# Kernel optimization log

Hardware: AMD Instinct MI355X
Metric: run time of the kernel (lower is better)

## Reference

```python
import jax, jax.numpy as jnp
import numpy as np

N = 50000        # nodes
E = 800000       # edges (before self loops)
NFEAT = 128
HEADS = 8
NHID = 16
SLOPE = 0.2      # PyG GATConv default negative_slope


def gat_conv(x, src, dst, W, a_src, a_dst, bias, heads, out_ch, concat):
    n = x.shape[0]
    h = (x @ W).reshape(n, heads, out_ch)                 # [N,H,C]
    al_s = jnp.sum(h * a_src, axis=-1)                    # [N,H]
    al_d = jnp.sum(h * a_dst, axis=-1)                    # [N,H]
    # add self loops (PyG GATConv default add_self_loops=True)
    loop = jnp.arange(n, dtype=src.dtype)
    s = jnp.concatenate([src, loop])
    d = jnp.concatenate([dst, loop])
    e = jax.nn.leaky_relu(al_s[s] + al_d[d], SLOPE)       # [E+N,H]
    # numerically stable softmax over incoming edges of each dst node
    emax = jax.lax.stop_gradient(jax.ops.segment_max(e, d, num_segments=n))
    ex = jnp.exp(e - emax[d])
    denom = jax.ops.segment_sum(ex, d, num_segments=n)
    alpha = ex / denom[d]                                 # [E+N,H]
    out = jax.ops.segment_sum(h[s] * alpha[:, :, None], d, num_segments=n)  # [N,H,C]
    out = out.reshape(n, heads * out_ch) if concat else out.mean(axis=1)
    return out + bias


def setup_inputs() -> dict:
    key = jax.random.key(0)
    ks = jax.random.split(key, 11)
    x = jax.random.normal(ks[0], (N, NFEAT), jnp.float32)
    src = jax.random.randint(ks[1], (E,), 0, N, dtype=jnp.int32)
    dst = jax.random.randint(ks[2], (E,), 0, N, dtype=jnp.int32)
    dst = jnp.where(src == dst, (dst + 1) % N, dst)  # no pre-existing self loops
    edge_index = jnp.stack([src, dst])
    sc = 0.1
    W1 = jax.random.normal(ks[3], (NFEAT, HEADS * NHID), jnp.float32) * sc
    a_src1 = jax.random.normal(ks[4], (HEADS, NHID), jnp.float32) * sc
    a_dst1 = jax.random.normal(ks[5], (HEADS, NHID), jnp.float32) * sc
    b1 = jnp.zeros((HEADS * NHID,), jnp.float32)
    W2 = jax.random.normal(ks[6], (HEADS * NHID, NHID), jnp.float32) * sc
    a_src2 = jax.random.normal(ks[7], (1, NHID), jnp.float32) * sc
    a_dst2 = jax.random.normal(ks[8], (1, NHID), jnp.float32) * sc
    b2 = jnp.zeros((NHID,), jnp.float32)
    return {"x": x, "edge_index": edge_index, "W1": W1, "a_src1": a_src1,
            "a_dst1": a_dst1, "b1": b1, "W2": W2, "a_src2": a_src2,
            "a_dst2": a_dst2, "b2": b2}


def reference(x, edge_index, W1, a_src1, a_dst1, b1, W2, a_src2, a_dst2, b2):
    src, dst = edge_index[0], edge_index[1]
    # layer 1: GATConv(nfeat -> nhid, heads=8, concat) + relu (dropout off in eval)
    h = jax.nn.relu(gat_conv(x, src, dst, W1, a_src1, a_dst1, b1, HEADS, NHID, True))
    # layer 2: GATConv(heads*nhid -> nhid, heads=1, concat=False) + relu
    out = jax.nn.relu(gat_conv(h, src, dst, W2, a_src2, a_dst2, b2, 1, NHID, False))
    return out
```

## Files before the change

kernel.cpp:

```cpp
#include <hip/hip_runtime.h>

#define NFEAT 128
#define HEADS 8
#define NHID 16
#define SLOPE 0.2f
#define BSH 8
#define CAPSH 13

typedef __fp16 f16x8 __attribute__((ext_vector_type(8)));
typedef __fp16 f16x2 __attribute__((ext_vector_type(2)));
typedef float  f4v   __attribute__((ext_vector_type(4)));

__device__ __forceinline__ unsigned pack2h(float a, float b) {
    union { f16x2 h; unsigned u; } r;
    r.h = __builtin_amdgcn_cvt_pkrtz(a, b);
    return r.u;
}
__device__ __forceinline__ f16x2 as_f16x2(unsigned u) {
    union { unsigned u; f16x2 h; } r; r.u = u; return r.h;
}
__device__ __forceinline__ f16x8 frag_from_f32(const float* p) {
    float4 q0 = *(const float4*)p;
    float4 q1 = *(const float4*)(p + 4);
    union { f16x8 v; f16x2 h[4]; } r;
    r.h[0] = __builtin_amdgcn_cvt_pkrtz(q0.x, q0.y);
    r.h[1] = __builtin_amdgcn_cvt_pkrtz(q0.z, q0.w);
    r.h[2] = __builtin_amdgcn_cvt_pkrtz(q1.x, q1.y);
    r.h[3] = __builtin_amdgcn_cvt_pkrtz(q1.z, q1.w);
    return r.v;
}


__global__ __launch_bounds__(256) void k_bscatter(const int* __restrict__ src,
                                                  const int* __restrict__ dst,
                                                  int E, int chunk,
                                                  int* __restrict__ bcount,
                                                  unsigned* __restrict__ pairs) {
    __shared__ int cnt[256], base[256];
    int t = threadIdx.x;
    int beg = blockIdx.x * chunk;
    int end = min(beg + chunk, E);
    if (beg >= end) return;
    cnt[t] = 0;
    __syncthreads();
    for (int i = beg + t; i < end; i += 256)
        atomicAdd(&cnt[dst[i] >> BSH], 1);
    __syncthreads();
    int c = cnt[t];
    base[t] = c ? (atomicAdd(&bcount[t], c) + (t << CAPSH)) : 0;
    __syncthreads();
    cnt[t] = 0;
    __syncthreads();
    for (int i = beg + t; i < end; i += 256) {
        int d = dst[i];
        int b = d >> BSH;
        int ofs = atomicAdd(&cnt[b], 1);
        pairs[base[b] + ofs] = (unsigned)src[i] | ((unsigned)(d & 255) << 16);
    }
}


__global__ __launch_bounds__(256) void k_scan_prep(const int* __restrict__ bcount,
                                                   int* __restrict__ cstart,
                                                   int* __restrict__ row_start,
                                                   int E, int n,
                                                   const float* __restrict__ W1,
                                                   const float* __restrict__ as1,
                                                   const float* __restrict__ ad1,
                                                   const float* __restrict__ W2,
                                                   unsigned* __restrict__ Wt1,
                                                   __fp16* __restrict__ Aat1,
                                                   unsigned* __restrict__ W2t) {
    if (blockIdx.x == 0) {
        __shared__ int sh[256];
        int t = threadIdx.x;
        int nb = (n + 255) >> BSH;
        int v = (t < nb) ? bcount[t] : 0;
        sh[t] = v;
        __syncthreads();
        for (int off = 1; off < 256; off <<= 1) {
            int u = (t >= off) ? sh[t - off] : 0;
            __syncthreads();
            sh[t] += u;
            __syncthreads();
        }
        cstart[t] = sh[t] - v;
        if (t == 0) row_start[n] = E + n;
        return;
    }
    int t = (blockIdx.x - 1) * 256 + threadIdx.x;
    if (t < 8192) {
        int c = t >> 6, m = t & 63;
        int k = 2 * m;
        Wt1[t] = pack2h(W1[k * 128 + c], W1[(k + 1) * 128 + c]);
    } else if (t < 10240) {
        int idx = t - 8192;
        int j = idx >> 7, k = idx & 127;
        float v = 0.f;
        if (j < 8)  { if ((k >> 4) == j)     v = as1[k]; }
        else        { if ((k >> 4) == j - 8) v = ad1[k]; }
        Aat1[idx] = (__fp16)v;
    } else if (t < 11264) {
        int idx = t - 10240;
        int c = idx >> 6, m = idx & 63;
        int k = 2 * m;
        W2t[idx] = pack2h(W2[k * 16 + c], W2[(k + 1) * 16 + c]);
    }
}


__global__ __launch_bounds__(256) void k_csr_gemm1(const unsigned* __restrict__ pairs,
                                                   const int* __restrict__ bcount,
                                                   const int* __restrict__ cstart,
                                                   int* __restrict__ row_start,
                                                   unsigned short* __restrict__ csr,
                                                   const float* __restrict__ xf,
                                                   const __fp16* __restrict__ Wt,
                                                   const __fp16* __restrict__ Aat,
                                                   unsigned* __restrict__ h1u,
                                                   float* __restrict__ als,
                                                   float* __restrict__ ald,
                                                   int n, int nbuck) {
    __shared__ unsigned smem[4][32 * 64];
    if ((int)blockIdx.x < nbuck) {
        int* deg = (int*)&smem[0][0];
        int* sc  = deg + 256;
        int b = blockIdx.x, t = threadIdx.x;
        int d0 = b << BSH;
        int nd = min(256, n - d0);
        deg[t] = (t < nd) ? 1 : 0;
        __syncthreads();
        int pbeg = b << CAPSH, pend = pbeg + bcount[b];
        for (int i = pbeg + t; i < pend; i += 256)
            atomicAdd(&deg[(pairs[i] >> 16) & 255], 1);
        __syncthreads();
        int v = deg[t];
        sc[t] = v;
        __syncthreads();
        for (int off = 1; off < 256; off <<= 1) {
            int u = (t >= off) ? sc[t - off] : 0;
            __syncthreads();
            sc[t] += u;
            __syncthreads();
        }
        int excl = sc[t] - v;
        int cbase = cstart[b] + d0;
        if (t < nd) row_start[d0 + t] = cbase + excl;
        __syncthreads();
        deg[t] = excl;
        __syncthreads();
        if (t < nd) {
            int pos = atomicAdd(&deg[t], 1);
            csr[cbase + pos] = (unsigned short)(d0 + t);
        }
        for (int i = pbeg + t; i < pend; i += 256) {
            unsigned p = pairs[i];
            int pos = atomicAdd(&deg[(p >> 16) & 255], 1);
            csr[cbase + pos] = (unsigned short)(p & 0xFFFFu);
        }
        return;
    }
    int bid = blockIdx.x - nbuck;
    int tid = threadIdx.x;
    int w = tid >> 6, l = tid & 63;
    int l15 = l & 15, lq = l >> 4;
    int wbase = bid * 128 + w * 32;
    f4v acc[2][8] = {};
    int r0 = min(wbase + l15, n - 1);
    int r1 = min(wbase + 16 + l15, n - 1);
#pragma unroll
    for (int kb = 0; kb < 4; ++kb) {
        int ko = kb * 32 + lq * 8;
        f16x8 a0 = frag_from_f32(&xf[(size_t)r0 * 128 + ko]);
        f16x8 a1 = frag_from_f32(&xf[(size_t)r1 * 128 + ko]);
#pragma unroll
        for (int cg = 0; cg < 8; ++cg) {
            f16x8 b = *(const f16x8*)&Wt[(size_t)(cg * 16 + l15) * 128 + ko];
            acc[0][cg] = __builtin_amdgcn_mfma_f32_16x16x32_f16(a0, b, acc[0][cg], 0, 0, 0);
            acc[1][cg] = __builtin_amdgcn_mfma_f32_16x16x32_f16(a1, b, acc[1][cg], 0, 0, 0);
        }
    }
    unsigned* myl = smem[w];
#pragma unroll
    for (int T = 0; T < 2; ++T) {
#pragma unroll
        for (int cg = 0; cg < 8; ++cg) {
#pragma unroll
            for (int j = 0; j < 4; ++j) {
                float v = acc[T][cg][j];
                float vo = __shfl_xor(v, 1);
                if ((l15 & 1) == 0) {
                    int nd = T * 16 + lq * 4 + j;
                    int wd = cg * 8 + (l15 >> 1);
                    int widx = nd * 64 + (((wd >> 2) ^ (nd & 15)) << 2) + (wd & 3);
                    myl[widx] = pack2h(v, vo);
                }
            }
        }
    }
    __syncthreads();
#pragma unroll
    for (int it = 0; it < 8; ++it) {
        int nd = it * 4 + lq;
        int node = wbase + nd;
        uint4 vv = *(const uint4*)&myl[nd * 64 + ((l15 ^ (nd & 15)) << 2)];
        if (node < n) *(uint4*)&h1u[(size_t)node * 64 + l15 * 4] = vv;
    }
#pragma unroll
    for (int T = 0; T < 2; ++T) {
        f4v acca = {};
#pragma unroll
        for (int kb = 0; kb < 4; ++kb) {
            int nd = T * 16 + l15;
            f16x8 ah = *(const f16x8*)&myl[nd * 64 + (((kb * 4 + lq) ^ (nd & 15)) << 2)];
            f16x8 bb = *(const f16x8*)&Aat[l15 * 128 + kb * 32 + lq * 8];
            acca = __builtin_amdgcn_mfma_f32_16x16x32_f16(ah, bb, acca, 0, 0, 0);
        }
#pragma unroll
        for (int j = 0; j < 4; ++j) {
            int node = wbase + T * 16 + lq * 4 + j;
            if (node < n) {
                if (l15 < 8) als[(size_t)node * 8 + l15] = acca[j];
                else         ald[(size_t)node * 8 + (l15 - 8)] = acca[j];
            }
        }
    }
}


__global__ __launch_bounds__(256) void k_agg1(const unsigned* __restrict__ hu,
                                              const float* __restrict__ als,
                                              const float* __restrict__ ald,
                                              const float* __restrict__ bias,
                                              const int* __restrict__ row_start,
                                              const unsigned short* __restrict__ csr,
                                              unsigned* __restrict__ out1u, int n) {
    int t = threadIdx.x;
    int w = t >> 6;
    int l = t & 63;
    int lc = l & 3;
    int es = (l >> 2) & 3;
    int ns = l >> 4;
    int g = blockIdx.x & 3;
    int nn = (blockIdx.x >> 2) * 16 + w * 4 + ns;
    if (nn >= n) return;
    const unsigned* hg = hu + g * 16;
    int hd = g * 2 + (lc >> 1);
    float aldv = ald[(size_t)nn * 8 + hd];
    int beg = row_start[nn], end = row_start[nn + 1];
    int len = end - beg;
    int g0 = beg + ((len * es) >> 2);
    int g1 = beg + ((len * (es + 1)) >> 2);
    float a[8] = {0.f, 0.f, 0.f, 0.f, 0.f, 0.f, 0.f, 0.f};
    float dn = 0.f;
    f16x2 one2; one2[0] = (__fp16)1.f; one2[1] = (__fp16)1.f;
    int i = g0;
    for (; i + 4 <= g1; i += 4) {
        int s0 = csr[i], s1 = csr[i + 1], s2 = csr[i + 2], s3 = csr[i + 3];
        float e0 = als[(size_t)s0 * 8 + hd];
        float e1 = als[(size_t)s1 * 8 + hd];
        float e2 = als[(size_t)s2 * 8 + hd];
        float e3 = als[(size_t)s3 * 8 + hd];
        uint4 v0 = *(const uint4*)&hg[(size_t)s0 * 64 + lc * 4];
        uint4 v1 = *(const uint4*)&hg[(size_t)s1 * 64 + lc * 4];
        uint4 v2 = *(const uint4*)&hg[(size_t)s2 * 64 + lc * 4];
        uint4 v3 = *(const uint4*)&hg[(size_t)s3 * 64 + lc * 4];
        e0 += aldv; e0 = (e0 < 0.f) ? SLOPE * e0 : e0;
        e1 += aldv; e1 = (e1 < 0.f) ? SLOPE * e1 : e1;
        e2 += aldv; e2 = (e2 < 0.f) ? SLOPE * e2 : e2;
        e3 += aldv; e3 = (e3 < 0.f) ? SLOPE * e3 : e3;
        f16x2 xa = __builtin_amdgcn_cvt_pkrtz(__expf(e0), __expf(e1));
        f16x2 xb = __builtin_amdgcn_cvt_pkrtz(__expf(e2), __expf(e3));
        dn = __builtin_amdgcn_fdot2(xa, one2, dn, false);
        dn = __builtin_amdgcn_fdot2(xb, one2, dn, false);
        unsigned V0[4] = {v0.x, v0.y, v0.z, v0.w};
        unsigned V1[4] = {v1.x, v1.y, v1.z, v1.w};
        unsigned V2[4] = {v2.x, v2.y, v2.z, v2.w};
        unsigned V3[4] = {v3.x, v3.y, v3.z, v3.w};
#pragma unroll
        for (int j = 0; j < 4; ++j) {
            unsigned lo01 = __builtin_amdgcn_perm(V1[j], V0[j], 0x05040100u);
            unsigned hi01 = __builtin_amdgcn_perm(V1[j], V0[j], 0x07060302u);
            unsigned lo23 = __builtin_amdgcn_perm(V3[j], V2[j], 0x05040100u);
            unsigned hi23 = __builtin_amdgcn_perm(V3[j], V2[j], 0x07060302u);
            a[2 * j]     = __builtin_amdgcn_fdot2(xa, as_f16x2(lo01), a[2 * j], false);
            a[2 * j + 1] = __builtin_amdgcn_fdot2(xa, as_f16x2(hi01), a[2 * j + 1], false);
            a[2 * j]     = __builtin_amdgcn_fdot2(xb, as_f16x2(lo23), a[2 * j], false);
            a[2 * j + 1] = __builtin_amdgcn_fdot2(xb, as_f16x2(hi23), a[2 * j + 1], false);
        }
    }
    for (; i + 2 <= g1; i += 2) {
        int s0 = csr[i];
        int s1 = csr[i + 1];
        float e0 = als[(size_t)s0 * 8 + hd];
        float e1 = als[(size_t)s1 * 8 + hd];
        uint4 v0 = *(const uint4*)&hg[(size_t)s0 * 64 + lc * 4];
        uint4 v1 = *(const uint4*)&hg[(size_t)s1 * 64 + lc * 4];
        e0 += aldv; e0 = (e0 < 0.f) ? SLOPE * e0 : e0;
        e1 += aldv; e1 = (e1 < 0.f) ? SLOPE * e1 : e1;
        f16x2 xx = __builtin_amdgcn_cvt_pkrtz(__expf(e0), __expf(e1));
        dn = __builtin_amdgcn_fdot2(xx, one2, dn, false);
        unsigned V0[4] = {v0.x, v0.y, v0.z, v0.w};
        unsigned V1[4] = {v1.x, v1.y, v1.z, v1.w};
#pragma unroll
        for (int j = 0; j < 4; ++j) {
            unsigned lo = __builtin_amdgcn_perm(V1[j], V0[j], 0x05040100u);
            unsigned hi = __builtin_amdgcn_perm(V1[j], V0[j], 0x07060302u);
            a[2 * j]     = __builtin_amdgcn_fdot2(xx, as_f16x2(lo), a[2 * j], false);
            a[2 * j + 1] = __builtin_amdgcn_fdot2(xx, as_f16x2(hi), a[2 * j + 1], false);
        }
    }
    if (i < g1) {
        int s0 = csr[i];
        float e0 = als[(size_t)s0 * 8 + hd] + aldv;
        uint4 v0 = *(const uint4*)&hg[(size_t)s0 * 64 + lc * 4];
        e0 = (e0 < 0.f) ? SLOPE * e0 : e0;
        float x0 = __expf(e0);
        dn += x0;
        unsigned V0[4] = {v0.x, v0.y, v0.z, v0.w};
#pragma unroll
        for (int j = 0; j < 4; ++j) {
            f16x2 p = as_f16x2(V0[j]);
            a[2 * j]     = fmaf(x0, (float)p[0], a[2 * j]);
            a[2 * j + 1] = fmaf(x0, (float)p[1], a[2 * j + 1]);
        }
    }
#pragma unroll
    for (int j = 0; j < 8; ++j) {
        a[j] += __shfl_xor(a[j], 4);
        a[j] += __shfl_xor(a[j], 8);
    }
    dn += __shfl_xor(dn, 4);
    dn += __shfl_xor(dn, 8);
    if (es == 0) {
        float inv = 1.f / dn;
        int ch = g * 32 + lc * 8;
        float4 b0 = *(const float4*)&bias[ch];
        float4 b1 = *(const float4*)&bias[ch + 4];
        uint4 o;
        o.x = pack2h(fmaxf(a[0] * inv + b0.x, 0.f), fmaxf(a[1] * inv + b0.y, 0.f));
        o.y = pack2h(fmaxf(a[2] * inv + b0.z, 0.f), fmaxf(a[3] * inv + b0.w, 0.f));
        o.z = pack2h(fmaxf(a[4] * inv + b1.x, 0.f), fmaxf(a[5] * inv + b1.y, 0.f));
        o.w = pack2h(fmaxf(a[6] * inv + b1.z, 0.f), fmaxf(a[7] * inv + b1.w, 0.f));
        *(uint4*)&out1u[(size_t)nn * 64 + g * 16 + lc * 4] = o;
    }
}


__global__ __launch_bounds__(256) void k_gemm2m(const __fp16* __restrict__ o1,
                                                const __fp16* __restrict__ W2t,
                                                const float* __restrict__ as2,
                                                const float* __restrict__ ad2,
                                                __fp16* __restrict__ h2,
                                                float* __restrict__ als,
                                                float* __restrict__ ald, int n) {
    int tid = threadIdx.x;
    int w = tid >> 6, l = tid & 63;
    int l15 = l & 15, lq = l >> 4;
    int wbase = blockIdx.x * 128 + w * 32;
    f4v acc[2] = {};
    int r0 = min(wbase + l15, n - 1);
    int r1 = min(wbase + 16 + l15, n - 1);
#pragma unroll
    for (int kb = 0; kb < 4; ++kb) {
        int ko = kb * 32 + lq * 8;
        f16x8 a0 = *(const f16x8*)&o1[(size_t)r0 * 128 + ko];
        f16x8 a1 = *(const f16x8*)&o1[(size_t)r1 * 128 + ko];
        f16x8 b  = *(const f16x8*)&W2t[(size_t)l15 * 128 + ko];
        acc[0] = __builtin_amdgcn_mfma_f32_16x16x32_f16(a0, b, acc[0], 0, 0, 0);
        acc[1] = __builtin_amdgcn_mfma_f32_16x16x32_f16(a1, b, acc[1], 0, 0, 0);
    }
    float asv = as2[l15], adv = ad2[l15];
#pragma unroll
    for (int T = 0; T < 2; ++T) {
#pragma unroll
        for (int j = 0; j < 4; ++j) {
            int node = wbase + T * 16 + lq * 4 + j;
            float hv = acc[T][j];
            float ps = hv * asv, pd = hv * adv;
            ps += __shfl_xor(ps, 1); ps += __shfl_xor(ps, 2);
            ps += __shfl_xor(ps, 4); ps += __shfl_xor(ps, 8);
            pd += __shfl_xor(pd, 1); pd += __shfl_xor(pd, 2);
            pd += __shfl_xor(pd, 4); pd += __shfl_xor(pd, 8);
            if (node < n) {
                h2[(size_t)node * 16 + l15] = (__fp16)hv;
                if (l15 == 0) { als[node] = ps; ald[node] = pd; }
            }
        }
    }
}


__global__ __launch_bounds__(256) void k_agg2(const __fp16* __restrict__ h,
                                              const float* __restrict__ als,
                                              const float* __restrict__ ald,
                                              const float* __restrict__ bias,
                                              const int* __restrict__ row_start,
                                              const unsigned short* __restrict__ csr,
                                              float* __restrict__ out, int n) {
    int t = threadIdx.x;
    int l = t & 63;
    int lc = l & 15, eg = l >> 4;
    int nn = blockIdx.x * 4 + (t >> 6);
    if (nn >= n) return;
    int beg = row_start[nn], end = row_start[nn + 1];
    int len = end - beg;
    int g0 = beg + ((len * eg) >> 2);
    int g1 = beg + ((len * (eg + 1)) >> 2);
    float aldv = ald[nn];
    float ac0 = 0.f, ac1 = 0.f, ac2 = 0.f, ac3 = 0.f;
    float dn0 = 0.f, dn1 = 0.f, dn2 = 0.f, dn3 = 0.f;
    int i = g0;
    for (; i + 4 <= g1; i += 4) {
        int s0 = csr[i], s1 = csr[i + 1], s2 = csr[i + 2], s3 = csr[i + 3];
        float e0 = als[s0], e1 = als[s1], e2 = als[s2], e3 = als[s3];
        float v0 = (float)h[(size_t)s0 * 16 + lc];
        float v1 = (float)h[(size_t)s1 * 16 + lc];
        float v2 = (float)h[(size_t)s2 * 16 + lc];
        float v3 = (float)h[(size_t)s3 * 16 + lc];
        e0 += aldv; e0 = (e0 < 0.f) ? SLOPE * e0 : e0;
        e1 += aldv; e1 = (e1 < 0.f) ? SLOPE * e1 : e1;
        e2 += aldv; e2 = (e2 < 0.f) ? SLOPE * e2 : e2;
        e3 += aldv; e3 = (e3 < 0.f) ? SLOPE * e3 : e3;
        float x0 = __expf(e0), x1 = __expf(e1), x2 = __expf(e2), x3 = __expf(e3);
        dn0 += x0; dn1 += x1; dn2 += x2; dn3 += x3;
        ac0 = fmaf(x0, v0, ac0);
        ac1 = fmaf(x1, v1, ac1);
        ac2 = fmaf(x2, v2, ac2);
        ac3 = fmaf(x3, v3, ac3);
    }
    for (; i < g1; ++i) {
        int s0 = csr[i];
        float e0 = als[s0] + aldv;
        e0 = (e0 < 0.f) ? SLOPE * e0 : e0;
        float x0 = __expf(e0);
        dn0 += x0;
        ac0 = fmaf(x0, (float)h[(size_t)s0 * 16 + lc], ac0);
    }
    float ac = (ac0 + ac1) + (ac2 + ac3);
    float dn = (dn0 + dn1) + (dn2 + dn3);
    ac += __shfl_xor(ac, 16); ac += __shfl_xor(ac, 32);
    dn += __shfl_xor(dn, 16); dn += __shfl_xor(dn, 32);
    if (eg == 0) out[(size_t)nn * 16 + lc] = fmaxf(ac / dn + bias[lc], 0.f);
}


extern "C" void kernel_launch(void* const* d_in, const int* in_sizes, int n_in,
                              void* d_out, int out_size, void* d_ws, size_t ws_size,
                              hipStream_t stream) {
    const float* x   = (const float*)d_in[0];
    const int*   ei  = (const int*)d_in[1];
    const float* W1  = (const float*)d_in[2];
    const float* as1 = (const float*)d_in[3];
    const float* ad1 = (const float*)d_in[4];
    const float* b1  = (const float*)d_in[5];
    const float* W2  = (const float*)d_in[6];
    const float* as2 = (const float*)d_in[7];
    const float* ad2 = (const float*)d_in[8];
    const float* b2  = (const float*)d_in[9];

    int N = in_sizes[0] / NFEAT;
    int E = in_sizes[1] / 2;
    const int* srcp = ei;
    const int* dstp = ei + E;
    int NBUCK = (N + 255) >> BSH;
    int NBg = (N + 127) / 128;

    char* ws = (char*)d_ws;
    size_t off = 0;
    auto take = [&](size_t bytes) -> char* {
        char* p = ws + off;
        off = (off + bytes + 255) & ~(size_t)255;
        return p;
    };
    int*            row_start = (int*)take((size_t)(N + 1) * 4);
    int*            bcount    = (int*)take(256 * 4);
    int*            cstart    = (int*)take(256 * 4);
    unsigned*       pairs     = (unsigned*)take((size_t)256 << (CAPSH + 2));
    unsigned short* csr       = (unsigned short*)take((size_t)(E + N) * 2);
    unsigned*       Wt1       = (unsigned*)take((size_t)128 * 64 * 4);
    __fp16*         Aat1      = (__fp16*)take((size_t)16 * 128 * 2);
    unsigned*       W2t       = (unsigned*)take((size_t)16 * 64 * 4);
    unsigned*       h1u       = (unsigned*)take((size_t)N * 64 * 4);
    float*          als1      = (float*)take((size_t)N * 8 * 4);
    float*          ald1      = (float*)take((size_t)N * 8 * 4);
    unsigned*       out1u     = (unsigned*)take((size_t)N * 64 * 4);
    __fp16*         h2        = (__fp16*)take((size_t)N * 16 * 2);
    float*          als2      = (float*)take((size_t)N * 4);
    float*          ald2      = (float*)take((size_t)N * 4);

    hipMemsetAsync(bcount, 0, 256 * 4, stream);
    int chunk = (E + 255) / 256;
    k_bscatter<<<256, 256, 0, stream>>>(srcp, dstp, E, chunk, bcount, pairs);
    k_scan_prep<<<45, 256, 0, stream>>>(bcount, cstart, row_start, E, N,
                                        W1, as1, ad1, W2, Wt1, Aat1, W2t);
    k_csr_gemm1<<<NBUCK + NBg, 256, 0, stream>>>(pairs, bcount, cstart, row_start, csr,
                                                 x, (const __fp16*)Wt1, Aat1,
                                                 h1u, als1, ald1, N, NBUCK);
    int nb1 = ((N + 15) / 16) * 4;
    k_agg1<<<nb1, 256, 0, stream>>>(h1u, als1, ald1, b1, row_start, csr, out1u, N);
    k_gemm2m<<<NBg, 256, 0, stream>>>((const __fp16*)out1u, (const __fp16*)W2t,
                                      as2, ad2, h2, als2, ald2, N);
    k_agg2<<<(N + 3) / 4, 256, 0, stream>>>(h2, als2, ald2, b2, row_start, csr, (float*)d_out, N);
}
```

Before: 135.4 us.

## Store layer-1 features and source logits head-major for per-head aggregation

The first GEMM kernel now writes h1 and the source attention logits head-major: one contiguous slice per head (32 bytes per node for features, one float per node for logits). The layer-1 aggregation is rebuilt so each block handles a single head for 32 nodes, with 2 lanes per head and the shuffle reductions adjusted to match. The goal is to shrink each head-group's working set so gathers over random source nodes get better cache locality, and to make logit gathers contiguous per head. In exchange there are twice as many blocks, each gather is narrower, and the CSR indices are read by 8 head-blocks instead of 4.

```diff
diff --git a/kernel.cpp b/kernel.cpp
--- a/kernel.cpp
+++ b/kernel.cpp
@@ -117,8 +117,8 @@
                                                    const float* __restrict__ xf,
                                                    const __fp16* __restrict__ Wt,
                                                    const __fp16* __restrict__ Aat,
-                                                   unsigned* __restrict__ h1u,
-                                                   float* __restrict__ als,
+                                                   unsigned* __restrict__ h1o,
+                                                   float* __restrict__ als_s,
                                                    float* __restrict__ ald,
                                                    int n, int nbuck) {
     __shared__ unsigned smem[4][32 * 64];
@@ -165,6 +165,7 @@
     int w = tid >> 6, l = tid & 63;
     int l15 = l & 15, lq = l >> 4;
     int wbase = bid * 128 + w * 32;
+    size_t oslice = (size_t)n * 8;
     f4v acc[2][8] = {};
     int r0 = min(wbase + l15, n - 1);
     int r1 = min(wbase + 16 + l15, n - 1);
@@ -204,7 +205,8 @@
         int nd = it * 4 + lq;
         int node = wbase + nd;
         uint4 vv = *(const uint4*)&myl[nd * 64 + ((l15 ^ (nd & 15)) << 2)];
-        if (node < n) *(uint4*)&h1u[(size_t)node * 64 + l15 * 4] = vv;
+        if (node < n)
+            *(uint4*)&h1o[(size_t)(l15 >> 1) * oslice + (size_t)node * 8 + (l15 & 1) * 4] = vv;
     }
 #pragma unroll
     for (int T = 0; T < 2; ++T) {
@@ -220,7 +222,7 @@
         for (int j = 0; j < 4; ++j) {
             int node = wbase + T * 16 + lq * 4 + j;
             if (node < n) {
-                if (l15 < 8) als[(size_t)node * 8 + l15] = acca[j];
+                if (l15 < 8) als_s[(size_t)l15 * n + node] = acca[j];
                 else         ald[(size_t)node * 8 + (l15 - 8)] = acca[j];
             }
         }
@@ -228,8 +230,8 @@
 }
 
 
-__global__ __launch_bounds__(256) void k_agg1(const unsigned* __restrict__ hu,
-                                              const float* __restrict__ als,
+__global__ __launch_bounds__(256) void k_agg1(const unsigned* __restrict__ h1o,
+                                              const float* __restrict__ als_s,
                                               const float* __restrict__ ald,
                                               const float* __restrict__ bias,
                                               const int* __restrict__ row_start,
@@ -238,15 +240,16 @@
     int t = threadIdx.x;
     int w = t >> 6;
     int l = t & 63;
-    int lc = l & 3;
-    int es = (l >> 2) & 3;
-    int ns = l >> 4;
-    int g = blockIdx.x & 3;
-    int nn = (blockIdx.x >> 2) * 16 + w * 4 + ns;
+    int lc = l & 1;
+    int es = (l >> 1) & 3;
+    int ns = l >> 3;
+    int g = blockIdx.x & 7;
+    int nn = (blockIdx.x >> 3) * 32 + w * 8 + ns;
     if (nn >= n) return;
-    const unsigned* hg = hu + g * 16;
-    int hd = g * 2 + (lc >> 1);
-    float aldv = ald[(size_t)nn * 8 + hd];
+    size_t oslice = (size_t)n * 8;
+    const unsigned* hg = h1o + (size_t)g * oslice;
+    const float* ag = als_s + (size_t)g * n;
+    float aldv = ald[(size_t)nn * 8 + g];
     int beg = row_start[nn], end = row_start[nn + 1];
     int len = end - beg;
     int g0 = beg + ((len * es) >> 2);
@@ -257,14 +260,14 @@
     int i = g0;
     for (; i + 4 <= g1; i += 4) {
         int s0 = csr[i], s1 = csr[i + 1], s2 = csr[i + 2], s3 = csr[i + 3];
-        float e0 = als[(size_t)s0 * 8 + hd];
-        float e1 = als[(size_t)s1 * 8 + hd];
-        float e2 = als[(size_t)s2 * 8 + hd];
-        float e3 = als[(size_t)s3 * 8 + hd];
-        uint4 v0 = *(const uint4*)&hg[(size_t)s0 * 64 + lc * 4];
-        uint4 v1 = *(const uint4*)&hg[(size_t)s1 * 64 + lc * 4];
-        uint4 v2 = *(const uint4*)&hg[(size_t)s2 * 64 + lc * 4];
-        uint4 v3 = *(const uint4*)&hg[(size_t)s3 * 64 + lc * 4];
+        float e0 = ag[s0];
+        float e1 = ag[s1];
+        float e2 = ag[s2];
+        float e3 = ag[s3];
+        uint4 v0 = *(const uint4*)&hg[(size_t)s0 * 8 + lc * 4];
+        uint4 v1 = *(const uint4*)&hg[(size_t)s1 * 8 + lc * 4];
+        uint4 v2 = *(const uint4*)&hg[(size_t)s2 * 8 + lc * 4];
+        uint4 v3 = *(const uint4*)&hg[(size_t)s3 * 8 + lc * 4];
         e0 += aldv; e0 = (e0 < 0.f) ? SLOPE * e0 : e0;
         e1 += aldv; e1 = (e1 < 0.f) ? SLOPE * e1 : e1;
         e2 += aldv; e2 = (e2 < 0.f) ? SLOPE * e2 : e2;
@@ -292,10 +295,10 @@
     for (; i + 2 <= g1; i += 2) {
         int s0 = csr[i];
         int s1 = csr[i + 1];
-        float e0 = als[(size_t)s0 * 8 + hd];
-        float e1 = als[(size_t)s1 * 8 + hd];
-        uint4 v0 = *(const uint4*)&hg[(size_t)s0 * 64 + lc * 4];
-        uint4 v1 = *(const uint4*)&hg[(size_t)s1 * 64 + lc * 4];
+        float e0 = ag[s0];
+        float e1 = ag[s1];
+        uint4 v0 = *(const uint4*)&hg[(size_t)s0 * 8 + lc * 4];
+        uint4 v1 = *(const uint4*)&hg[(size_t)s1 * 8 + lc * 4];
         e0 += aldv; e0 = (e0 < 0.f) ? SLOPE * e0 : e0;
         e1 += aldv; e1 = (e1 < 0.f) ? SLOPE * e1 : e1;
         f16x2 xx = __builtin_amdgcn_cvt_pkrtz(__expf(e0), __expf(e1));
@@ -312,8 +315,8 @@
     }
     if (i < g1) {
         int s0 = csr[i];
-        float e0 = als[(size_t)s0 * 8 + hd] + aldv;
-        uint4 v0 = *(const uint4*)&hg[(size_t)s0 * 64 + lc * 4];
+        float e0 = ag[s0] + aldv;
+        uint4 v0 = *(const uint4*)&hg[(size_t)s0 * 8 + lc * 4];
         e0 = (e0 < 0.f) ? SLOPE * e0 : e0;
         float x0 = __expf(e0);
         dn += x0;
@@ -327,14 +330,14 @@
     }
 #pragma unroll
     for (int j = 0; j < 8; ++j) {
+        a[j] += __shfl_xor(a[j], 2);
         a[j] += __shfl_xor(a[j], 4);
-        a[j] += __shfl_xor(a[j], 8);
-    }
+    }
+    dn += __shfl_xor(dn, 2);
     dn += __shfl_xor(dn, 4);
-    dn += __shfl_xor(dn, 8);
     if (es == 0) {
         float inv = 1.f / dn;
-        int ch = g * 32 + lc * 8;
+        int ch = g * 16 + lc * 8;
         float4 b0 = *(const float4*)&bias[ch];
         float4 b1 = *(const float4*)&bias[ch + 4];
         uint4 o;
@@ -342,7 +345,7 @@
         o.y = pack2h(fmaxf(a[2] * inv + b0.z, 0.f), fmaxf(a[3] * inv + b0.w, 0.f));
         o.z = pack2h(fmaxf(a[4] * inv + b1.x, 0.f), fmaxf(a[5] * inv + b1.y, 0.f));
         o.w = pack2h(fmaxf(a[6] * inv + b1.z, 0.f), fmaxf(a[7] * inv + b1.w, 0.f));
-        *(uint4*)&out1u[(size_t)nn * 64 + g * 16 + lc * 4] = o;
+        *(uint4*)&out1u[(size_t)nn * 64 + g * 8 + lc * 4] = o;
     }
 }
 
@@ -481,8 +484,8 @@
     unsigned*       Wt1       = (unsigned*)take((size_t)128 * 64 * 4);
     __fp16*         Aat1      = (__fp16*)take((size_t)16 * 128 * 2);
     unsigned*       W2t       = (unsigned*)take((size_t)16 * 64 * 4);
-    unsigned*       h1u       = (unsigned*)take((size_t)N * 64 * 4);
-    float*          als1      = (float*)take((size_t)N * 8 * 4);
+    unsigned*       h1o       = (unsigned*)take((size_t)N * 64 * 4);
+    float*          als_s     = (float*)take((size_t)N * 8 * 4);
     float*          ald1      = (float*)take((size_t)N * 8 * 4);
     unsigned*       out1u     = (unsigned*)take((size_t)N * 64 * 4);
     __fp16*         h2        = (__fp16*)take((size_t)N * 16 * 2);
@@ -496,9 +499,9 @@
                                         W1, as1, ad1, W2, Wt1, Aat1, W2t);
     k_csr_gemm1<<<NBUCK + NBg, 256, 0, stream>>>(pairs, bcount, cstart, row_start, csr,
                                                  x, (const __fp16*)Wt1, Aat1,
-                                                 h1u, als1, ald1, N, NBUCK);
-    int nb1 = ((N + 15) / 16) * 4;
-    k_agg1<<<nb1, 256, 0, stream>>>(h1u, als1, ald1, b1, row_start, csr, out1u, N);
+                                                 h1o, als_s, ald1, N, NBUCK);
+    int nb1 = ((N + 31) / 32) * 8;
+    k_agg1<<<nb1, 256, 0, stream>>>(h1o, als_s, ald1, b1, row_start, csr, out1u, N);
     k_gemm2m<<<NBg, 256, 0, stream>>>((const __fp16*)out1u, (const __fp16*)W2t,
                                       as2, ad2, h2, als2, ald2, N);
     k_agg2<<<(N + 3) / 4, 256, 0, stream>>>(h2, als2, ald2, b2, row_start, csr, (float*)d_out, N);
```

Measured after the change: 137.0 us. No clear change (+1.2%).
